# Optimization experiments

Measured on AMD Instinct MI355X. Metric: run time of the kernel, lower is better.

Reference implementation:

```python
import jax, jax.numpy as jnp
import numpy as np

BN_EPS = 1e-5


def _conv_bn_elu(x, w, b, bn_scale, bn_bias, bn_mean, bn_var):
    # 1x1 conv == channel-mixing matmul: x [B,C,H,W], w [O,C]
    y = jnp.einsum('bchw,oc->bohw', x, w) + b[None, :, None, None]
    inv = bn_scale * jax.lax.rsqrt(bn_var + BN_EPS)
    y = y * inv[None, :, None, None] + (bn_bias - bn_mean * inv)[None, :, None, None]
    return jax.nn.elu(y)


def setup_inputs() -> dict:
    key = jax.random.key(0)
    ks = jax.random.split(key, 24)
    B, C, H, W = 4, 128, 64, 64
    d = {}
    d['x_q'] = jax.random.normal(ks[0], (B, C, H, W), jnp.float32)
    d['x_k'] = jax.random.normal(ks[1], (B, C, H, W), jnp.float32)
    d['x_v'] = jax.random.normal(ks[2], (B, C, H, W), jnp.float32)
    scale = 1.0 / np.sqrt(C)
    i = 3
    for p in ('q', 'k', 'v'):
        d[f'{p}_w'] = jax.random.normal(ks[i], (C, C), jnp.float32) * scale; i += 1
        d[f'{p}_b'] = jax.random.normal(ks[i], (C,), jnp.float32) * 0.01; i += 1
        d[f'{p}_bn_scale'] = jnp.ones((C,), jnp.float32) + 0.1 * jax.random.normal(ks[i], (C,), jnp.float32); i += 1
        d[f'{p}_bn_bias'] = 0.1 * jax.random.normal(ks[i], (C,), jnp.float32); i += 1
        d[f'{p}_bn_mean'] = 0.1 * jax.random.normal(ks[i], (C,), jnp.float32); i += 1
        d[f'{p}_bn_var'] = jax.random.uniform(ks[i], (C,), jnp.float32, 0.5, 1.5); i += 1
    # torch inits gamma/beta to zero; use small nonzero values so output is informative
    d['gamma'] = jnp.array([0.5], jnp.float32)
    d['beta'] = jnp.array([0.5], jnp.float32)
    return d


def reference(x_q, x_k, x_v,
              q_w, q_b, q_bn_scale, q_bn_bias, q_bn_mean, q_bn_var,
              k_w, k_b, k_bn_scale, k_bn_bias, k_bn_mean, k_bn_var,
              v_w, v_b, v_bn_scale, v_bn_bias, v_bn_mean, v_bn_var,
              gamma, beta):
    B, C, Hv, Wv = x_v.shape
    q = _conv_bn_elu(x_q, q_w, q_b, q_bn_scale, q_bn_bias, q_bn_mean, q_bn_var).reshape(B, C, -1)  # [B,C,HWq]
    k = _conv_bn_elu(x_k, k_w, k_b, k_bn_scale, k_bn_bias, k_bn_mean, k_bn_var).reshape(B, C, -1)  # [B,C,HWk]
    v = _conv_bn_elu(x_v, v_w, v_b, v_bn_scale, v_bn_bias, v_bn_mean, v_bn_var).reshape(B, C, -1)  # [B,C,HWv]
    energy = jnp.einsum('bcq,bck->bqk', q, k)                 # [B,HWq,HWk] (no scaling, as in source)
    attention = jax.nn.softmax(energy, axis=-1)
    out = jnp.einsum('bck,bqk->bcq', v, attention)            # [B,C,HWq]
    out = out.reshape(B, C, Hv, Wv)
    return gamma * out + beta * x_v
```

## Files before the change

### kernel.cpp

```cpp
#include <hip/hip_runtime.h>

#define CC 128
#define SS 4096
#define L2E 1.44269504f

typedef _Float16 f16;
typedef f16 f16x8 __attribute__((ext_vector_type(8)));
typedef float f32x4 __attribute__((ext_vector_type(4)));

struct PArg { const float *x, *w, *b, *sc, *bb, *bm, *bv; f16* out; };

__global__ __launch_bounds__(256) void projk(PArg A0, PArg A1, PArg A2) {
    const int p = blockIdx.y;
    PArg A = (p == 0) ? A0 : ((p == 1) ? A1 : A2);
    const int bx = blockIdx.x;
    const int b  = bx >> 6;
    const int s0 = (bx & 63) * 64;
    const int tid = threadIdx.x;
    const int w = tid >> 6, lane = tid & 63;
    const int n = lane & 15, g = lane >> 4;

    __shared__ f16 Xl[64][136];
    __shared__ f16 Wl[128][136];
    f16* Yl = &Wl[0][0];

#pragma unroll
    for (int i = 0; i < 8; ++i) {
        int vi = tid + i * 256;
        int c = vi >> 4, sq = (vi & 15) * 4;
        float4 v = *(const float4*)(A.x + ((size_t)b * CC + c) * SS + s0 + sq);
        Xl[sq + 0][c] = (f16)v.x; Xl[sq + 1][c] = (f16)v.y;
        Xl[sq + 2][c] = (f16)v.z; Xl[sq + 3][c] = (f16)v.w;
    }
#pragma unroll
    for (int i = 0; i < 8; ++i) {
        int vi = tid + i * 256;
        int o = vi >> 4, cq = (vi & 15) * 8;
        float iv = A.sc[o] * rsqrtf(A.bv[o] + 1e-5f);
        const float* wp = A.w + o * CC + cq;
        float4 a = *(const float4*)wp;
        float4 b4 = *(const float4*)(wp + 4);
        union { f16 h[8]; uint4 u; } pk;
        pk.h[0] = (f16)(a.x * iv);  pk.h[1] = (f16)(a.y * iv);
        pk.h[2] = (f16)(a.z * iv);  pk.h[3] = (f16)(a.w * iv);
        pk.h[4] = (f16)(b4.x * iv); pk.h[5] = (f16)(b4.y * iv);
        pk.h[6] = (f16)(b4.z * iv); pk.h[7] = (f16)(b4.w * iv);
        *(uint4*)&Wl[o][cq] = pk.u;
    }
    __syncthreads();

    if (p < 2) {
        f32x4 acc[2][4];
#pragma unroll
        for (int mt = 0; mt < 2; ++mt)
#pragma unroll
            for (int nt = 0; nt < 4; ++nt) acc[mt][nt] = (f32x4){0.f, 0.f, 0.f, 0.f};
#pragma unroll
        for (int ks = 0; ks < 4; ++ks) {
            f16x8 af[2], bf[4];
#pragma unroll
            for (int mt = 0; mt < 2; ++mt) af[mt] = *(const f16x8*)&Wl[w * 32 + mt * 16 + n][ks * 32 + g * 8];
#pragma unroll
            for (int nt = 0; nt < 4; ++nt) bf[nt] = *(const f16x8*)&Xl[nt * 16 + n][ks * 32 + g * 8];
#pragma unroll
            for (int mt = 0; mt < 2; ++mt)
#pragma unroll
                for (int nt = 0; nt < 4; ++nt)
                    acc[mt][nt] = __builtin_amdgcn_mfma_f32_16x16x32_f16(af[mt], bf[nt], acc[mt][nt], 0, 0, 0);
        }
        __syncthreads();
#pragma unroll
        for (int mt = 0; mt < 2; ++mt) {
            float ebr[4];
#pragma unroll
            for (int r = 0; r < 4; ++r) {
                int o = w * 32 + mt * 16 + g * 4 + r;
                float iv = A.sc[o] * rsqrtf(A.bv[o] + 1e-5f);
                ebr[r] = (A.b[o] - A.bm[o]) * iv + A.bb[o];
            }
#pragma unroll
            for (int nt = 0; nt < 4; ++nt) {
                union { f16 h[4]; uint2 u; } pk;
#pragma unroll
                for (int r = 0; r < 4; ++r) {
                    float y = acc[mt][nt][r] + ebr[r];
                    y = (y > 0.f) ? y : (__expf(y) - 1.f);
                    pk.h[r] = (f16)y;
                }
                *(uint2*)&Yl[(nt * 16 + n) * 136 + w * 32 + mt * 16 + g * 4] = pk.u;
            }
        }
        __syncthreads();
#pragma unroll
        for (int i = 0; i < 4; ++i) {
            int vi = tid + i * 256;
            int s = vi >> 4, cl = (vi & 15) * 8;
            *(uint4*)&A.out[((size_t)b * SS + s0 + s) * CC + cl] = *(const uint4*)&Yl[s * 136 + cl];
        }
    } else {
        f32x4 acc[8];
#pragma unroll
        for (int nt = 0; nt < 8; ++nt) acc[nt] = (f32x4){0.f, 0.f, 0.f, 0.f};
#pragma unroll
        for (int ks = 0; ks < 4; ++ks) {
            f16x8 af = *(const f16x8*)&Xl[w * 16 + n][ks * 32 + g * 8];
#pragma unroll
            for (int nt = 0; nt < 8; ++nt) {
                f16x8 bf = *(const f16x8*)&Wl[nt * 16 + n][ks * 32 + g * 8];
                acc[nt] = __builtin_amdgcn_mfma_f32_16x16x32_f16(af, bf, acc[nt], 0, 0, 0);
            }
        }
        __syncthreads();
#pragma unroll
        for (int nt = 0; nt < 8; ++nt) {
            int o = nt * 16 + n;
            float iv = A.sc[o] * rsqrtf(A.bv[o] + 1e-5f);
            float ebc = (A.b[o] - A.bm[o]) * iv + A.bb[o];
            union { f16 h[4]; uint2 u; } pk;
#pragma unroll
            for (int r = 0; r < 4; ++r) {
                float y = acc[nt][r] + ebc;
                y = (y > 0.f) ? y : (__expf(y) - 1.f);
                pk.h[r] = (f16)y;
            }
            *(uint2*)&Yl[(nt * 16 + n) * 136 + w * 16 + g * 4] = pk.u;
        }
        __syncthreads();
#pragma unroll
        for (int i = 0; i < 4; ++i) {
            int vi = tid + i * 256;
            int o = vi >> 3, sl = (vi & 7) * 8;
            *(uint4*)&A.out[((size_t)b * CC + o) * SS + s0 + sl] = *(const uint4*)&Yl[o * 136 + sl];
        }
    }
}

__global__ __launch_bounds__(256, 3) void attnk(
    const f16* __restrict__ Qt, const f16* __restrict__ Kt, const f16* __restrict__ Vt,
    f16* __restrict__ Op, float* __restrict__ Ml)
{
    const int tid = threadIdx.x;
    const int bx = blockIdx.x;
    const int kh = bx & 7;
    const int b  = (bx >> 3) & 3;
    const int qt = bx >> 5;
    const int q0 = qt * 128;
    const int kbeg = kh * 512;

    __shared__ __align__(16) char arena[48128];
    const int w = tid >> 6, lane = tid & 63;
    const int n = lane & 15, g = lane >> 4;
    f16 (*Pw)[40] = (f16(*)[40])(arena + 37888 + w * 2560);

    f16x8 qf[2][4];
    {
        const f16* Qb = Qt + ((size_t)b * SS + q0 + w * 32) * CC;
#pragma unroll
        for (int qt2 = 0; qt2 < 2; ++qt2)
#pragma unroll
            for (int ks = 0; ks < 4; ++ks)
                qf[qt2][ks] = *(const f16x8*)&Qb[(qt2 * 16 + n) * CC + ks * 32 + g * 8];
    }

    f32x4 oacc[8][2];
#pragma unroll
    for (int mtc = 0; mtc < 8; ++mtc)
#pragma unroll
        for (int qt2 = 0; qt2 < 2; ++qt2) oacc[mtc][qt2] = (f32x4){0.f, 0.f, 0.f, 0.f};
    float mreg[2] = {-1e30f, -1e30f}, lsum[2] = {0.f, 0.f};

    const int rk0 = tid >> 4,        ck0 = (tid & 15) * 8;
    const int rk1 = (tid + 256) >> 4, ck1 = ((tid + 256) & 15) * 8;
    const int rv0 = tid >> 2,        cv0 = (tid & 3) * 8;
    const int rv1 = (tid + 256) >> 2, cv1 = ((tid + 256) & 3) * 8;

    {
        f16 (*Kl)[136] = (f16(*)[136])(arena);
        f16 (*Vl)[40]  = (f16(*)[40])(arena + 17408);
        *(uint4*)&Kl[rk0][ck0] = *(const uint4*)&Kt[((size_t)b * SS + kbeg + rk0) * CC + ck0];
        *(uint4*)&Kl[rk1][ck1] = *(const uint4*)&Kt[((size_t)b * SS + kbeg + rk1) * CC + ck1];
        *(uint4*)&Vl[rv0][cv0] = *(const uint4*)&Vt[((size_t)b * CC + rv0) * SS + kbeg + cv0];
        *(uint4*)&Vl[rv1][cv1] = *(const uint4*)&Vt[((size_t)b * CC + rv1) * SS + kbeg + cv1];
    }

    for (int kt = 0; kt < 16; ++kt) {
        const int cur = kt & 1;
        f16 (*Kl)[136] = (f16(*)[136])(arena + cur * 8704);
        f16 (*Vl)[40]  = (f16(*)[40])(arena + 17408 + cur * 10240);
        f16 (*Kn)[136] = (f16(*)[136])(arena + (1 - cur) * 8704);
        f16 (*Vn)[40]  = (f16(*)[40])(arena + 17408 + (1 - cur) * 10240);

        __syncthreads();

        uint4 nk0, nk1, nv0, nv1;
        if (kt < 15) {
            const int k1 = kbeg + (kt + 1) * 32;
            nk0 = *(const uint4*)&Kt[((size_t)b * SS + k1 + rk0) * CC + ck0];
            nk1 = *(const uint4*)&Kt[((size_t)b * SS + k1 + rk1) * CC + ck1];
            nv0 = *(const uint4*)&Vt[((size_t)b * CC + rv0) * SS + k1 + cv0];
            nv1 = *(const uint4*)&Vt[((size_t)b * CC + rv1) * SS + k1 + cv1];
        }

        f32x4 sacc[2][2];
#pragma unroll
        for (int kt2 = 0; kt2 < 2; ++kt2)
#pragma unroll
            for (int qt2 = 0; qt2 < 2; ++qt2) sacc[kt2][qt2] = (f32x4){0.f, 0.f, 0.f, 0.f};
#pragma unroll
        for (int ks = 0; ks < 4; ++ks) {
            f16x8 kf[2];
#pragma unroll
            for (int kt2 = 0; kt2 < 2; ++kt2) kf[kt2] = *(const f16x8*)&Kl[kt2 * 16 + n][ks * 32 + g * 8];
#pragma unroll
            for (int kt2 = 0; kt2 < 2; ++kt2)
#pragma unroll
                for (int qt2 = 0; qt2 < 2; ++qt2)
                    sacc[kt2][qt2] = __builtin_amdgcn_mfma_f32_16x16x32_f16(kf[kt2], qf[qt2][ks], sacc[kt2][qt2], 0, 0, 0);
        }

        if (kt < 15) {
            *(uint4*)&Kn[rk0][ck0] = nk0;
            *(uint4*)&Kn[rk1][ck1] = nk1;
            *(uint4*)&Vn[rv0][cv0] = nv0;
            *(uint4*)&Vn[rv1][cv1] = nv1;
        }

        float al[2];
#pragma unroll
        for (int qt2 = 0; qt2 < 2; ++qt2) {
            float v = sacc[0][qt2][0];
#pragma unroll
            for (int kt2 = 0; kt2 < 2; ++kt2)
#pragma unroll
                for (int r = 0; r < 4; ++r) v = fmaxf(v, sacc[kt2][qt2][r]);
            v = fmaxf(v, __shfl_xor(v, 16));
            v = fmaxf(v, __shfl_xor(v, 32));
            float mn = fmaxf(mreg[qt2], v);
            al[qt2] = exp2f((mreg[qt2] - mn) * L2E);
            mreg[qt2] = mn;
            float rs = 0.f;
#pragma unroll
            for (int kt2 = 0; kt2 < 2; ++kt2) {
                union { f16 h[4]; uint2 u; } pk;
#pragma unroll
                for (int r = 0; r < 4; ++r) {
                    float p = exp2f((sacc[kt2][qt2][r] - mn) * L2E);
                    rs += p;
                    pk.h[r] = (f16)p;
                }
                *(uint2*)&Pw[qt2 * 16 + n][kt2 * 16 + g * 4] = pk.u;
            }
            lsum[qt2] = lsum[qt2] * al[qt2] + rs;
        }
#pragma unroll
        for (int mtc = 0; mtc < 8; ++mtc)
#pragma unroll
            for (int qt2 = 0; qt2 < 2; ++qt2)
#pragma unroll
                for (int r = 0; r < 4; ++r) oacc[mtc][qt2][r] *= al[qt2];

        {
            f16x8 pf[2];
#pragma unroll
            for (int qt2 = 0; qt2 < 2; ++qt2) pf[qt2] = *(const f16x8*)&Pw[qt2 * 16 + n][g * 8];
#pragma unroll
            for (int mtc = 0; mtc < 8; ++mtc) {
                f16x8 vf = *(const f16x8*)&Vl[mtc * 16 + n][g * 8];
#pragma unroll
                for (int qt2 = 0; qt2 < 2; ++qt2)
                    oacc[mtc][qt2] = __builtin_amdgcn_mfma_f32_16x16x32_f16(vf, pf[qt2], oacc[mtc][qt2], 0, 0, 0);
            }
        }
    }

    float lreg[2];
#pragma unroll
    for (int qt2 = 0; qt2 < 2; ++qt2) {
        float s = lsum[qt2];
        s += __shfl_xor(s, 16);
        s += __shfl_xor(s, 32);
        lreg[qt2] = s;
    }

    const int pidx = (b * 32 + qt) * 8 + kh;
    if (g == 0) {
        float* MlW = Ml + (size_t)pidx * 256;
#pragma unroll
        for (int qt2 = 0; qt2 < 2; ++qt2) {
            int q = w * 32 + qt2 * 16 + n;
            MlW[q]       = mreg[qt2];
            MlW[128 + q] = lreg[qt2];
        }
    }

    __syncthreads();
    f16 (*S2)[136] = (f16(*)[136])arena;
#pragma unroll
    for (int mtc = 0; mtc < 8; ++mtc)
#pragma unroll
        for (int qt2 = 0; qt2 < 2; ++qt2)
#pragma unroll
            for (int r = 0; r < 4; ++r)
                S2[mtc * 16 + g * 4 + r][w * 32 + qt2 * 16 + n] = (f16)oacc[mtc][qt2][r];
    __syncthreads();
    f16* OpW = Op + (size_t)pidx * 16384;
#pragma unroll
    for (int i = 0; i < 8; ++i) {
        int vi = tid + i * 256;
        int c = vi >> 4, qq = (vi & 15) * 8;
        *(uint4*)&OpW[c * 128 + qq] = *(const uint4*)&S2[c][qq];
    }
}

__global__ __launch_bounds__(256) void mrgk(
    const f16* __restrict__ Op, const float* __restrict__ Ml,
    const float* __restrict__ xv, const float* __restrict__ gp, const float* __restrict__ bp,
    float* __restrict__ out)
{
    const int bx = blockIdx.x;
    const int cg = bx & 3, bqt = bx >> 2;
    const int b = bqt >> 5, qt = bqt & 31;
    const int tid = threadIdx.x;
    const int q = tid & 127, hf = tid >> 7;

    const float* ml = Ml + (size_t)bqt * 8 * 256;
    float m = -1e30f;
#pragma unroll
    for (int k2 = 0; k2 < 8; ++k2) m = fmaxf(m, ml[k2 * 256 + q]);
    float wt[8], tot = 0.f;
#pragma unroll
    for (int k2 = 0; k2 < 8; ++k2) {
        wt[k2] = exp2f((ml[k2 * 256 + q] - m) * L2E);
        tot += wt[k2] * ml[k2 * 256 + 128 + q];
    }
    float inv = 1.f / tot;
    float gm = gp[0], bb = bp[0];

    const f16* O = Op + (size_t)bqt * 8 * 16384;
#pragma unroll 2
    for (int i = 0; i < 16; ++i) {
        int c = cg * 32 + hf * 16 + i;
        float o = 0.f;
#pragma unroll
        for (int k2 = 0; k2 < 8; ++k2) o += wt[k2] * (float)O[k2 * 16384 + c * 128 + q];
        o *= inv;
        size_t idx = ((size_t)(b * CC + c)) * SS + qt * 128 + q;
        out[idx] = gm * o + bb * xv[idx];
    }
}

extern "C" void kernel_launch(void* const* d_in, const int* in_sizes, int n_in,
                              void* d_out, int out_size, void* d_ws, size_t ws_size,
                              hipStream_t stream) {
    (void)in_sizes; (void)n_in; (void)out_size; (void)ws_size;

    const size_t TEN = (size_t)4 * SS * CC;
    f16* Qt = (f16*)d_ws;
    f16* Kt = Qt + TEN;
    f16* Vt = Kt + TEN;
    f16* Op = Vt + TEN;
    float* Ml = (float*)(Op + (size_t)1024 * 16384);

    PArg aq = { (const float*)d_in[0], (const float*)d_in[3],  (const float*)d_in[4],
                (const float*)d_in[5], (const float*)d_in[6],  (const float*)d_in[7],
                (const float*)d_in[8],  Qt };
    PArg ak = { (const float*)d_in[1], (const float*)d_in[9],  (const float*)d_in[10],
                (const float*)d_in[11], (const float*)d_in[12], (const float*)d_in[13],
                (const float*)d_in[14], Kt };
    PArg av = { (const float*)d_in[2], (const float*)d_in[15], (const float*)d_in[16],
                (const float*)d_in[17], (const float*)d_in[18], (const float*)d_in[19],
                (const float*)d_in[20], Vt };

    hipLaunchKernelGGL(projk, dim3(256, 3), dim3(256), 0, stream, aq, ak, av);
    hipLaunchKernelGGL(attnk, dim3(1024), dim3(256), 0, stream, Qt, Kt, Vt, Op, Ml);
    hipLaunchKernelGGL(mrgk, dim3(512), dim3(256), 0, stream,
                       Op, Ml, (const float*)d_in[2], (const float*)d_in[21],
                       (const float*)d_in[22], (float*)d_out);
}
```

Baseline: 187.9 us.

## Fold log2e into Q, swizzle K smem, shrink LDS for higher occupancy

The Q projection now pre-multiplies its output by log2(e), so the attention and merge kernels can call exp2 directly without a per-element multiply. K tiles in shared memory switch from padded rows to an XOR-swizzled layout, and V/P tiles drop their padding. Together these shrink the LDS arena so the launch bound can rise from 3 to 4 blocks per CU. The change also adds s_setprio around the MFMA loops and packs probabilities with cvt_pkrtz. Risks: unpadded V/P rows may cause bank conflicts, rounding toward zero slightly changes precision, and the tighter occupancy bound may cause register spills.

```diff
diff --git a/kernel.cpp b/kernel.cpp
--- a/kernel.cpp
+++ b/kernel.cpp
@@ -6,6 +6,7 @@
 
 typedef _Float16 f16;
 typedef f16 f16x8 __attribute__((ext_vector_type(8)));
+typedef __fp16 h16x2 __attribute__((ext_vector_type(2)));
 typedef float f32x4 __attribute__((ext_vector_type(4)));
 
 struct PArg { const float *x, *w, *b, *sc, *bb, *bm, *bv; f16* out; };
@@ -50,6 +51,7 @@
     __syncthreads();
 
     if (p < 2) {
+        const float qsc = (p == 0) ? L2E : 1.0f;
         f32x4 acc[2][4];
 #pragma unroll
         for (int mt = 0; mt < 2; ++mt)
@@ -85,7 +87,7 @@
                 for (int r = 0; r < 4; ++r) {
                     float y = acc[mt][nt][r] + ebr[r];
                     y = (y > 0.f) ? y : (__expf(y) - 1.f);
-                    pk.h[r] = (f16)y;
+                    pk.h[r] = (f16)(y * qsc);
                 }
                 *(uint2*)&Yl[(nt * 16 + n) * 136 + w * 32 + mt * 16 + g * 4] = pk.u;
             }
@@ -135,7 +137,11 @@
     }
 }
 
-__global__ __launch_bounds__(256, 3) void attnk(
+__device__ __forceinline__ void* kg(char* base, int row, int c16) {
+    return base + row * 256 + (((c16) ^ (row & 7)) << 4);
+}
+
+__global__ __launch_bounds__(256, 4) void attnk(
     const f16* __restrict__ Qt, const f16* __restrict__ Kt, const f16* __restrict__ Vt,
     f16* __restrict__ Op, float* __restrict__ Ml)
 {
@@ -147,10 +153,10 @@
     const int q0 = qt * 128;
     const int kbeg = kh * 512;
 
-    __shared__ __align__(16) char arena[48128];
+    __shared__ __align__(16) char arena[40960];
     const int w = tid >> 6, lane = tid & 63;
     const int n = lane & 15, g = lane >> 4;
-    f16 (*Pw)[40] = (f16(*)[40])(arena + 37888 + w * 2560);
+    char* Pb = arena + 32768 + w * 2048;
 
     f16x8 qf[2][4];
     {
@@ -169,36 +175,38 @@
         for (int qt2 = 0; qt2 < 2; ++qt2) oacc[mtc][qt2] = (f32x4){0.f, 0.f, 0.f, 0.f};
     float mreg[2] = {-1e30f, -1e30f}, lsum[2] = {0.f, 0.f};
 
-    const int rk0 = tid >> 4,        ck0 = (tid & 15) * 8;
-    const int rk1 = (tid + 256) >> 4, ck1 = ((tid + 256) & 15) * 8;
-    const int rv0 = tid >> 2,        cv0 = (tid & 3) * 8;
-    const int rv1 = (tid + 256) >> 2, cv1 = ((tid + 256) & 3) * 8;
+    const int rk0 = tid >> 4, c16k = tid & 15;
+    const int rv0 = tid >> 2, cvg  = tid & 3;
 
     {
-        f16 (*Kl)[136] = (f16(*)[136])(arena);
-        f16 (*Vl)[40]  = (f16(*)[40])(arena + 17408);
-        *(uint4*)&Kl[rk0][ck0] = *(const uint4*)&Kt[((size_t)b * SS + kbeg + rk0) * CC + ck0];
-        *(uint4*)&Kl[rk1][ck1] = *(const uint4*)&Kt[((size_t)b * SS + kbeg + rk1) * CC + ck1];
-        *(uint4*)&Vl[rv0][cv0] = *(const uint4*)&Vt[((size_t)b * CC + rv0) * SS + kbeg + cv0];
-        *(uint4*)&Vl[rv1][cv1] = *(const uint4*)&Vt[((size_t)b * CC + rv1) * SS + kbeg + cv1];
+        char* Kb = arena;
+        char* Vb = arena + 16384;
+        const f16* Ksrc = Kt + ((size_t)b * SS + kbeg) * CC;
+        const f16* Vsrc = Vt + (size_t)b * CC * SS + kbeg;
+        *(uint4*)kg(Kb, rk0,      c16k) = *(const uint4*)&Ksrc[rk0 * CC + c16k * 8];
+        *(uint4*)kg(Kb, rk0 + 16, c16k) = *(const uint4*)&Ksrc[(rk0 + 16) * CC + c16k * 8];
+        *(uint4*)(Vb + rv0 * 64 + cvg * 16)        = *(const uint4*)&Vsrc[(size_t)rv0 * SS + cvg * 8];
+        *(uint4*)(Vb + (rv0 + 64) * 64 + cvg * 16) = *(const uint4*)&Vsrc[(size_t)(rv0 + 64) * SS + cvg * 8];
     }
 
     for (int kt = 0; kt < 16; ++kt) {
         const int cur = kt & 1;
-        f16 (*Kl)[136] = (f16(*)[136])(arena + cur * 8704);
-        f16 (*Vl)[40]  = (f16(*)[40])(arena + 17408 + cur * 10240);
-        f16 (*Kn)[136] = (f16(*)[136])(arena + (1 - cur) * 8704);
-        f16 (*Vn)[40]  = (f16(*)[40])(arena + 17408 + (1 - cur) * 10240);
+        char* Kb = arena + cur * 8192;
+        char* Vb = arena + 16384 + cur * 8192;
+        char* Kn = arena + (1 - cur) * 8192;
+        char* Vn = arena + 16384 + (1 - cur) * 8192;
 
         __syncthreads();
 
         uint4 nk0, nk1, nv0, nv1;
         if (kt < 15) {
             const int k1 = kbeg + (kt + 1) * 32;
-            nk0 = *(const uint4*)&Kt[((size_t)b * SS + k1 + rk0) * CC + ck0];
-            nk1 = *(const uint4*)&Kt[((size_t)b * SS + k1 + rk1) * CC + ck1];
-            nv0 = *(const uint4*)&Vt[((size_t)b * CC + rv0) * SS + k1 + cv0];
-            nv1 = *(const uint4*)&Vt[((size_t)b * CC + rv1) * SS + k1 + cv1];
+            const f16* Ksrc = Kt + ((size_t)b * SS + k1) * CC;
+            const f16* Vsrc = Vt + (size_t)b * CC * SS + k1;
+            nk0 = *(const uint4*)&Ksrc[rk0 * CC + c16k * 8];
+            nk1 = *(const uint4*)&Ksrc[(rk0 + 16) * CC + c16k * 8];
+            nv0 = *(const uint4*)&Vsrc[(size_t)rv0 * SS + cvg * 8];
+            nv1 = *(const uint4*)&Vsrc[(size_t)(rv0 + 64) * SS + cvg * 8];
         }
 
         f32x4 sacc[2][2];
@@ -206,49 +214,51 @@
         for (int kt2 = 0; kt2 < 2; ++kt2)
 #pragma unroll
             for (int qt2 = 0; qt2 < 2; ++qt2) sacc[kt2][qt2] = (f32x4){0.f, 0.f, 0.f, 0.f};
+        __builtin_amdgcn_s_setprio(1);
 #pragma unroll
         for (int ks = 0; ks < 4; ++ks) {
             f16x8 kf[2];
-#pragma unroll
-            for (int kt2 = 0; kt2 < 2; ++kt2) kf[kt2] = *(const f16x8*)&Kl[kt2 * 16 + n][ks * 32 + g * 8];
+            kf[0] = *(const f16x8*)kg(Kb, n,      ks * 4 + g);
+            kf[1] = *(const f16x8*)kg(Kb, 16 + n, ks * 4 + g);
 #pragma unroll
             for (int kt2 = 0; kt2 < 2; ++kt2)
 #pragma unroll
                 for (int qt2 = 0; qt2 < 2; ++qt2)
                     sacc[kt2][qt2] = __builtin_amdgcn_mfma_f32_16x16x32_f16(kf[kt2], qf[qt2][ks], sacc[kt2][qt2], 0, 0, 0);
         }
+        __builtin_amdgcn_s_setprio(0);
 
         if (kt < 15) {
-            *(uint4*)&Kn[rk0][ck0] = nk0;
-            *(uint4*)&Kn[rk1][ck1] = nk1;
-            *(uint4*)&Vn[rv0][cv0] = nv0;
-            *(uint4*)&Vn[rv1][cv1] = nv1;
+            *(uint4*)kg(Kn, rk0,      c16k) = nk0;
+            *(uint4*)kg(Kn, rk0 + 16, c16k) = nk1;
+            *(uint4*)(Vn + rv0 * 64 + cvg * 16)        = nv0;
+            *(uint4*)(Vn + (rv0 + 64) * 64 + cvg * 16) = nv1;
         }
 
         float al[2];
 #pragma unroll
         for (int qt2 = 0; qt2 < 2; ++qt2) {
-            float v = sacc[0][qt2][0];
-#pragma unroll
-            for (int kt2 = 0; kt2 < 2; ++kt2)
-#pragma unroll
-                for (int r = 0; r < 4; ++r) v = fmaxf(v, sacc[kt2][qt2][r]);
+            float v = fmaxf(fmaxf(fmaxf(sacc[0][qt2][0], sacc[0][qt2][1]),
+                                  fmaxf(sacc[0][qt2][2], sacc[0][qt2][3])),
+                            fmaxf(fmaxf(sacc[1][qt2][0], sacc[1][qt2][1]),
+                                  fmaxf(sacc[1][qt2][2], sacc[1][qt2][3])));
             v = fmaxf(v, __shfl_xor(v, 16));
             v = fmaxf(v, __shfl_xor(v, 32));
             float mn = fmaxf(mreg[qt2], v);
-            al[qt2] = exp2f((mreg[qt2] - mn) * L2E);
+            al[qt2] = exp2f(mreg[qt2] - mn);
             mreg[qt2] = mn;
             float rs = 0.f;
 #pragma unroll
             for (int kt2 = 0; kt2 < 2; ++kt2) {
-                union { f16 h[4]; uint2 u; } pk;
-#pragma unroll
-                for (int r = 0; r < 4; ++r) {
-                    float p = exp2f((sacc[kt2][qt2][r] - mn) * L2E);
-                    rs += p;
-                    pk.h[r] = (f16)p;
-                }
-                *(uint2*)&Pw[qt2 * 16 + n][kt2 * 16 + g * 4] = pk.u;
+                float p0 = exp2f(sacc[kt2][qt2][0] - mn);
+                float p1 = exp2f(sacc[kt2][qt2][1] - mn);
+                float p2 = exp2f(sacc[kt2][qt2][2] - mn);
+                float p3 = exp2f(sacc[kt2][qt2][3] - mn);
+                rs += (p0 + p1) + (p2 + p3);
+                union { h16x2 h[2]; uint2 u; } pk;
+                pk.h[0] = __builtin_amdgcn_cvt_pkrtz(p0, p1);
+                pk.h[1] = __builtin_amdgcn_cvt_pkrtz(p2, p3);
+                *(uint2*)(Pb + (qt2 * 16 + n) * 64 + kt2 * 32 + g * 8) = pk.u;
             }
             lsum[qt2] = lsum[qt2] * al[qt2] + rs;
         }
@@ -256,20 +266,21 @@
         for (int mtc = 0; mtc < 8; ++mtc)
 #pragma unroll
             for (int qt2 = 0; qt2 < 2; ++qt2)
-#pragma unroll
-                for (int r = 0; r < 4; ++r) oacc[mtc][qt2][r] *= al[qt2];
+                oacc[mtc][qt2] *= al[qt2];
 
         {
             f16x8 pf[2];
-#pragma unroll
-            for (int qt2 = 0; qt2 < 2; ++qt2) pf[qt2] = *(const f16x8*)&Pw[qt2 * 16 + n][g * 8];
+            pf[0] = *(const f16x8*)(Pb + n * 64 + g * 16);
+            pf[1] = *(const f16x8*)(Pb + (16 + n) * 64 + g * 16);
+            __builtin_amdgcn_s_setprio(1);
 #pragma unroll
             for (int mtc = 0; mtc < 8; ++mtc) {
-                f16x8 vf = *(const f16x8*)&Vl[mtc * 16 + n][g * 8];
+                f16x8 vf = *(const f16x8*)(Vb + (mtc * 16 + n) * 64 + g * 16);
 #pragma unroll
                 for (int qt2 = 0; qt2 < 2; ++qt2)
                     oacc[mtc][qt2] = __builtin_amdgcn_mfma_f32_16x16x32_f16(vf, pf[qt2], oacc[mtc][qt2], 0, 0, 0);
             }
+            __builtin_amdgcn_s_setprio(0);
         }
     }
 
@@ -330,7 +341,7 @@
     float wt[8], tot = 0.f;
 #pragma unroll
     for (int k2 = 0; k2 < 8; ++k2) {
-        wt[k2] = exp2f((ml[k2 * 256 + q] - m) * L2E);
+        wt[k2] = exp2f(ml[k2 * 256 + q] - m);
         tot += wt[k2] * ml[k2 * 256 + 128 + q];
     }
     float inv = 1.f / tot;
```

Result: slower. 267.4 us (+42.3%).
